# Performance work log

Hardware: AMD Instinct MI355X
Metric: run time of the kernel (lower is better)

## Reference

```python
import jax, jax.numpy as jnp
import numpy as np
from jax import lax

K = 5          # dynamic kernel size
GROUPS = 8     # inter_channels // group_channels = 128 // 16
R = 2          # pixel shuffle upscale factor
SLOPE = 0.01   # LeakyReLU default negative_slope
EPS = 1e-5     # BatchNorm eps


def conv2d(x, w, b, pad=0):
    # x: [B,C,H,W], w: [O,I,kh,kw]
    y = lax.conv_general_dilated(x, w, (1, 1), [(pad, pad), (pad, pad)],
                                 dimension_numbers=('NCHW', 'OIHW', 'NCHW'))
    return y + b[None, :, None, None]


def pixel_shuffle(x, r):
    B, C, H, W = x.shape
    x = x.reshape(B, C // (r * r), r, r, H, W)
    x = x.transpose(0, 1, 4, 2, 5, 3)  # B, C', H, r, W, r
    return x.reshape(B, C // (r * r), H * r, W * r)


def involution(x, weight, k, groups, pad):
    # x: [B,C,H,W]; weight: [B,groups,k,k,H,W]
    # out[b, g*gc+c, h, w] = sum_ij weight[b,g,i,j,h,w] * x_pad[b, g*gc+c, h+i, w+j]
    B, C, H, W = x.shape
    gc = C // groups
    xp = jnp.pad(x, ((0, 0), (0, 0), (pad, pad), (pad, pad)))
    xg = xp.reshape(B, groups, gc, H + 2 * pad, W + 2 * pad)
    out = jnp.zeros((B, groups, gc, H, W), x.dtype)
    for i in range(k):
        for j in range(k):
            out = out + weight[:, :, None, i, j] * xg[:, :, :, i:i + H, j:j + W]
    return out.reshape(B, C, H, W)


def setup_inputs() -> dict:
    key = jax.random.key(0)
    ks = jax.random.split(key, 16)
    s = 0.05
    return {
        'high_level': jax.random.normal(ks[0], (8, 128, 64, 64), jnp.float32),
        'low_level': jax.random.normal(ks[1], (8, 224, 128, 128), jnp.float32),
        'emb': jax.random.normal(ks[2], (8, 256, 128, 128), jnp.float32),
        'reduce_w': jax.random.normal(ks[3], (128, 256, 1, 1), jnp.float32) * s,
        'reduce_b': jax.random.normal(ks[4], (128,), jnp.float32) * s,
        'conv1_w': jax.random.normal(ks[5], (32, 128, 1, 1), jnp.float32) * s,
        'conv1_b': jax.random.normal(ks[6], (32,), jnp.float32) * s,
        'conv2_w': jax.random.normal(ks[7], (200, 32, 3, 3), jnp.float32) * s,
        'conv2_b': jax.random.normal(ks[8], (200,), jnp.float32) * s,
        'embconv_w': jax.random.normal(ks[9], (32, 256, 1, 1), jnp.float32) * s,
        'embconv_b': jax.random.normal(ks[10], (32,), jnp.float32) * s,
        'out_w': jax.random.normal(ks[11], (64, 128, 1, 1), jnp.float32) * s,
        'out_b': jax.random.normal(ks[12], (64,), jnp.float32) * s,
        'bn_gamma': jnp.ones((64,), jnp.float32),
        'bn_beta': jnp.zeros((64,), jnp.float32),
        'bn_mean': jnp.zeros((64,), jnp.float32),
        'bn_var': jax.random.uniform(ks[13], (64,), jnp.float32, 0.5, 1.5),
    }


def reference(high_level, low_level, emb,
              reduce_w, reduce_b, conv1_w, conv1_b, conv2_w, conv2_b,
              embconv_w, embconv_b, out_w, out_b,
              bn_gamma, bn_beta, bn_mean, bn_var):
    cat = jnp.concatenate([pixel_shuffle(high_level, R), low_level], axis=1)
    cat = conv2d(cat, reduce_w, reduce_b)
    mix = jax.nn.leaky_relu(conv2d(cat, conv1_w, conv1_b)
                            + conv2d(emb, embconv_w, embconv_b), SLOPE)
    w = conv2d(mix, conv2_w, conv2_b, pad=1)  # [B, K*K*GROUPS, H, W]
    B, _, H, W = w.shape
    w = w.reshape(B, GROUPS, K, K, H, W)
    o = involution(cat, w, K, GROUPS, (K - 1) // 2)
    o = conv2d(o, out_w, out_b)
    o = (o - bn_mean[None, :, None, None]) * (bn_gamma[None, :, None, None]
        / jnp.sqrt(bn_var[None, :, None, None] + EPS)) + bn_beta[None, :, None, None]
    return jax.nn.leaky_relu(o, SLOPE)
```

## Files before the change

kernel.cpp:

```cpp
#include <hip/hip_runtime.h>

typedef unsigned short u16; typedef unsigned int u32; typedef unsigned long long u64;
typedef __attribute__((ext_vector_type(8))) short short8;
typedef __attribute__((ext_vector_type(16))) float f32x16;

#define HW 16384

#define RED_B  0
#define C1E_B  128
#define C2_B   160
#define OUT_B  416
#define BN_SC  480
#define BN_SH  544
#define FLAG_OFF   4096
#define RWB_OFF    8192
#define C1B_OFF    73728
#define EMBB_OFF   81920
#define OUTB_OFF   98304
#define C2PB_OFF   114688
#define WEFF_OFF   262144
#define CAT2_OFF   524288
#define MIX_OFF    34078720

__device__ __forceinline__ float bf2f(u16 x){ u32 u=((u32)x)<<16; float f; __builtin_memcpy(&f,&u,4); return f; }
__device__ __forceinline__ u16 f2bf(float f){ u32 u; __builtin_memcpy(&u,&f,4); return (u16)((u + 0x7fffu + ((u>>16)&1u))>>16); }
__device__ __forceinline__ u32 pk2(float a, float b){ return (u32)f2bf(a) | ((u32)f2bf(b)<<16); }
__device__ __forceinline__ float lrelu(float x){ return x>0.f ? x : 0.01f*x; }

template<int M> __device__ __forceinline__ u16 ldb(const void* p, size_t i){
    if (M==1) return ((const u16*)p)[i];
    return f2bf(((const float*)p)[i]);
}
template<int M> __device__ __forceinline__ float ldf(const void* p, size_t i){
    if (M==1) return bf2f(((const u16*)p)[i]);
    return ((const float*)p)[i];
}
__device__ __forceinline__ int swz(int p){ return ((p>>1) ^ (p>>3)) & 7; }

__device__ __forceinline__ void gl16(const void* g, void* l){
    __builtin_amdgcn_global_load_lds(
        (const __attribute__((address_space(1))) u32*)g,
        (__attribute__((address_space(3))) u32*)l, 16, 0, 0);
}

__global__ void detect_kernel(const void* __restrict__ emb, u32* __restrict__ flag){
    int tid = threadIdx.x;
    const u16* p = (const u16*)emb;
    int e = (p[tid*2] >> 7) & 0xFF;
    u64 m = __ballot(e >= 100 && e <= 140);
    if (tid == 0) *flag = (__popcll(m) >= 32) ? 1u : 0u;
}

template<int M>
__device__ __forceinline__ void prep_body(
    const void* rw, const void* rb, const void* c1w, const void* c1b,
    const void* c2w, const void* c2b, const void* ew, const void* eb,
    const void* ow, const void* ob, const void* gam, const void* bet,
    const void* mn, const void* vr, char* ws)
{
    float* wf = (float*)ws;
    int i = blockIdx.x*256 + threadIdx.x;
    if (i < 32768) {
        int o = i>>8, ic = i&255;
        int s = ic>>4, qq = (ic>>3)&1, e = ic&7;
        int dst = (((o>>5)*16 + s)*64 + qq*32 + (o&31))*8 + e;
        ((u16*)(ws+RWB_OFF))[dst] = ldb<M>(rw, i);
    }
    else if (i < 36864)  ((u16*)(ws+C1B_OFF))[i-32768] = ldb<M>(c1w, i-32768);
    else if (i < 45056)  ((u16*)(ws+EMBB_OFF))[i-36864] = ldb<M>(ew, i-36864);
    else if (i < 53248)  ((u16*)(ws+OUTB_OFF))[i-45056] = ldb<M>(ow, i-45056);
    else if (i < 126976) {
        int j = i-53248; int o = j/288, k = j - o*288;
        int tap = k>>5, ic = k&31;
        u16 v = 0;
        if (o < 200) v = ldb<M>(c2w, (size_t)o*288 + ic*9 + tap);
        ((u16*)(ws+C2PB_OFF))[j] = v;
    }
    else if (i < 127584) {
        int j = i-126976;
        if (j < 128) wf[RED_B+j] = ldf<M>(rb, j);
        else if (j < 160) {
            int o = j-128;
            float s = ldf<M>(c1b,o) + ldf<M>(eb,o);
#pragma unroll 8
            for (int ic=0; ic<128; ic++)
                s += ldf<M>(c1w, (size_t)o*128+ic) * ldf<M>(rb, ic);
            wf[C1E_B+o] = s;
        }
        else if (j < 416) { int o = j-160; wf[C2_B+o] = (o<200) ? ldf<M>(c2b,o) : 0.f; }
        else if (j < 480) wf[OUT_B+j-416] = ldf<M>(ob, j-416);
        else if (j < 544) { int c=j-480; wf[BN_SC+c] = ldf<M>(gam,c) * rsqrtf(ldf<M>(vr,c)+1e-5f); }
        else { int c=j-544; wf[BN_SH+c] = ldf<M>(bet,c) - ldf<M>(mn,c)*ldf<M>(gam,c)*rsqrtf(ldf<M>(vr,c)+1e-5f); }
    }
    else if (i < 135776) {
        int j = i - 127584; int oc = j>>8, k2 = j&255;
        float s = 0.f;
#pragma unroll 8
        for (int ic=0; ic<128; ic++)
            s += ldf<M>(c1w, (size_t)oc*128+ic) * ldf<M>(rw, (size_t)ic*256+k2);
        ((u16*)(ws+WEFF_OFF))[oc*256+k2] = f2bf(s);
    }
}

__global__ __launch_bounds__(256) void k_prep(
    const void* rw, const void* rb, const void* c1w, const void* c1b,
    const void* c2w, const void* c2b, const void* ew, const void* eb,
    const void* ow, const void* ob, const void* gam, const void* bet,
    const void* mn, const void* vr, char* ws, const u32* __restrict__ flag)
{
    if (*flag) prep_body<1>(rw,rb,c1w,c1b,c2w,c2b,ew,eb,ow,ob,gam,bet,mn,vr,ws);
    else       prep_body<0>(rw,rb,c1w,c1b,c2w,c2b,ew,eb,ow,ob,gam,bet,mn,vr,ws);
}

__global__ __launch_bounds__(512) void k_rm(
    const void* __restrict__ hi, const void* __restrict__ lo, const void* __restrict__ emb,
    const u16* __restrict__ rwB, const u16* __restrict__ weffB, const u16* __restrict__ embB,
    const float* __restrict__ wf, u16* __restrict__ cat2, u16* __restrict__ mixt,
    const u32* __restrict__ flag)
{
    if (*flag != 1u) return;
    __shared__ u16 At1[64*264];
    __shared__ u16 At2[64*264];
    __shared__ u16 raw[34816];

    const int tid = threadIdx.x, wvi = tid>>6, lane = tid&63;
    const int col = lane&31, q = lane>>5;
    const int gpx = blockIdx.x*64;
    const int b = gpx>>14, p0 = gpx&16383;
    const int h = p0>>7, w0 = p0&127;

    {
        for (int i=wvi; i<28; i+=8){
            int chunk = i*64 + lane;
            int ch = chunk>>3, p8 = chunk&7;
            gl16((const u16*)lo + ((size_t)(b*224+ch))*HW + p0 + p8*8,
                 (char*)raw + i*1024);
        }
        {
            int i = wvi;
            int chunk = i*64 + lane;
            int hc = chunk>>2, c4 = chunk&3;
            gl16((const u16*)hi + ((size_t)(b*128+hc))*4096 + (size_t)(h>>1)*64 + (w0>>1) + c4*8,
                 (char*)raw + 28672 + i*1024);
        }
        for (int i=wvi; i<32; i+=8){
            int chunk = i*64 + lane;
            int ch = chunk>>3, p8 = chunk&7;
            gl16((const u16*)emb + ((size_t)(b*256+ch))*HW + p0 + p8*8,
                 (char*)raw + 36864 + i*1024);
        }
    }
    __syncthreads();

    {
        const int sthr = tid & 255;
        const int co = sthr>>3, po = sthr&7;
        u32 W[8][4];
        if (tid >= 256) {
            u32 R[8][4];
#pragma unroll
            for (int j=0;j<8;j++)
                __builtin_memcpy(&R[j][0], raw + 18432 + (8*co+j)*64 + po*8, 16);
#pragma unroll
            for (int p=0;p<8;p++){
                const int u = p>>1, hf = p&1;
#pragma unroll
                for (int m=0;m<4;m++){
                    u32 A0 = R[2*m][u], A1 = R[2*m+1][u];
                    W[p][m] = hf ? ((A0>>16) | (A1 & 0xffff0000u))
                                 : ((A0 & 0xffffu) | (A1<<16));
                }
            }
#pragma unroll
            for (int p=0;p<8;p++){
                int pg = 8*po + p;
                __builtin_memcpy(At2 + pg*264 + ((co ^ swz(pg))<<3), &W[p][0], 16);
            }
        } else if (co >= 4) {
            u32 R[8][4];
#pragma unroll
            for (int j=0;j<8;j++)
                __builtin_memcpy(&R[j][0], raw + (8*(co-4)+j)*64 + po*8, 16);
#pragma unroll
            for (int p=0;p<8;p++){
                const int u = p>>1, hf = p&1;
#pragma unroll
                for (int m=0;m<4;m++){
                    u32 A0 = R[2*m][u], A1 = R[2*m+1][u];
                    W[p][m] = hf ? ((A0>>16) | (A1 & 0xffff0000u))
                                 : ((A0 & 0xffffu) | (A1<<16));
                }
            }
#pragma unroll
            for (int p=0;p<8;p++){
                int pg = 8*po + p;
                __builtin_memcpy(At1 + pg*264 + ((co ^ swz(pg))<<3), &W[p][0], 16);
            }
        } else {
            const int h2 = (h&1)*2;
            u32 E[8][2], O[8][2];
#pragma unroll
            for (int j=0;j<8;j++){
                int hc = (8*co+j)*4 + h2;
                __builtin_memcpy(&E[j][0], raw + 14336 + hc*32 + po*4, 8);
                __builtin_memcpy(&O[j][0], raw + 14336 + (hc+1)*32 + po*4, 8);
            }
#pragma unroll
            for (int p=0;p<8;p++){
                const int k = p>>1, u = k>>1, hf = k&1;
#pragma unroll
                for (int m=0;m<4;m++){
                    u32 A0, A1;
                    if (p&1){ A0 = O[2*m][u]; A1 = O[2*m+1][u]; }
                    else    { A0 = E[2*m][u]; A1 = E[2*m+1][u]; }
                    W[p][m] = hf ? ((A0>>16) | (A1 & 0xffff0000u))
                                 : ((A0 & 0xffffu) | (A1<<16));
                }
            }
#pragma unroll
            for (int p=0;p<8;p++){
                int pg = 8*po + p;
                __builtin_memcpy(At1 + pg*264 + ((co ^ swz(pg))<<3), &W[p][0], 16);
            }
        }
    }
    __syncthreads();

    const int pt = wvi>>2, ks = wvi&3;
    const int pp = pt*32 + col, sw = swz(pp);
    const u16* arow1 = At1 + pp*264;
    const u16* arow2 = At2 + pp*264;

    f32x16 racc, macc;
#pragma unroll
    for (int r=0;r<16;r++){ racc[r]=0.f; macc[r]=0.f; }

    short8 Wf[4], Be2[4];
#pragma unroll
    for (int t4=0;t4<4;t4++)
        __builtin_memcpy(&Wf[t4], weffB + (size_t)col*256 + (4*ks+t4)*16 + q*8, 16);
#pragma unroll
    for (int t4=0;t4<4;t4++)
        __builtin_memcpy(&Be2[t4], embB + (size_t)col*256 + (4*ks+t4)*16 + q*8, 16);

#pragma unroll
    for (int bt=0; bt<4; bt++){
        short8 Bb[4];
#pragma unroll
        for (int si=0;si<4;si++)
            __builtin_memcpy(&Bb[si], rwB + (((size_t)(ks*16 + bt*4 + si))*64 + lane)*8, 16);
#pragma unroll
        for (int si=0;si<4;si++){
            int s = bt*4 + si;
            short8 a; __builtin_memcpy(&a, arow1 + (((2*s+q)^sw)<<3), 16);
            racc = __builtin_amdgcn_mfma_f32_32x32x16_bf16(a, Bb[si], racc, 0,0,0);
            int d = s - 4*ks;
            if (d>=0 && d<4)
                macc = __builtin_amdgcn_mfma_f32_32x32x16_bf16(a, Wf[d], macc, 0,0,0);
        }
    }
#pragma unroll
    for (int t4=0;t4<4;t4++){
        int t = 4*ks + t4;
        short8 a; __builtin_memcpy(&a, arow2 + (((2*t+q)^sw)<<3), 16);
        macc = __builtin_amdgcn_mfma_f32_32x32x16_bf16(a, Be2[t4], macc, 0,0,0);
    }
    {
        int oc = ks*32 + col;
        float bias = wf[RED_B + oc];
#pragma unroll
        for (int r=0;r<16;r++){
            int row = (r&3) + 8*(r>>2) + 4*q;
            cat2[((size_t)(gpx + pt*32 + row))*128 + oc] = f2bf(racc[r] + bias);
        }
    }

    float* exch = (float*)raw;
    if (ks != 0){
#pragma unroll
        for (int r=0;r<16;r++){
            int row = (r&3) + 8*(r>>2) + 4*q;
            exch[pt*3072 + (ks-1)*1024 + row*32 + col] = macc[r];
        }
    }
    __syncthreads();
    if (ks == 0){
        float bias = wf[C1E_B + col];
#pragma unroll
        for (int r=0;r<16;r++){
            int row = (r&3) + 8*(r>>2) + 4*q;
            int base = pt*3072 + row*32 + col;
            float v = macc[r] + exch[base] + exch[base+1024] + exch[base+2048] + bias;
            mixt[((size_t)(gpx + pt*32 + row))*32 + col] = f2bf(lrelu(v));
        }
    }
}

template<int M>
__device__ __forceinline__ void rm_body_reg(
    const void* __restrict__ hi, const void* __restrict__ lo, const void* __restrict__ emb,
    const u16* __restrict__ rwB, const u16* __restrict__ weffB, const u16* __restrict__ embB,
    const float* __restrict__ wf, u16* __restrict__ cat2, u16* __restrict__ mixt,
    u16* At)
{
    const int tid = threadIdx.x, wvi = tid>>6, lane = tid&63;
    const int col = lane&31, q = lane>>5;
    const int gpx = blockIdx.x*64;
    const int b = gpx>>14, p0 = gpx&16383;
    const int h = p0>>7, w0 = p0&127;

    const int sthr = tid & 255;
    const int co = sthr>>3, po = sthr&7;
    const bool is_emb = tid >= 256;

    u32 Wreg[8][4];

    if (is_emb) {
        u32 R[8][4];
        size_t base = ((size_t)(b*256 + 8*co))*HW + p0 + 8*po;
        float raw[8][8];
#pragma unroll
        for (int j=0;j<8;j++)
            __builtin_memcpy(&raw[j][0], (const float*)emb + base + (size_t)j*HW, 32);
#pragma unroll
        for (int j=0;j<8;j++)
#pragma unroll
        for (int m=0;m<4;m++) R[j][m] = pk2(raw[j][2*m], raw[j][2*m+1]);
#pragma unroll
        for (int p=0;p<8;p++){
            const int u = p>>1, hf = p&1;
#pragma unroll
            for (int m=0;m<4;m++){
                u32 A0 = R[2*m][u], A1 = R[2*m+1][u];
                Wreg[p][m] = hf ? ((A0>>16) | (A1 & 0xffff0000u))
                                : ((A0 & 0xffffu) | (A1<<16));
            }
        }
    } else {
        u32 W[8][4];
        if (co < 28) {
            u32 R[8][4];
            size_t base = ((size_t)(b*224 + 8*co))*HW + p0 + 8*po;
            float raw[8][8];
#pragma unroll
            for (int j=0;j<8;j++)
                __builtin_memcpy(&raw[j][0], (const float*)lo + base + (size_t)j*HW, 32);
#pragma unroll
            for (int j=0;j<8;j++)
#pragma unroll
            for (int m=0;m<4;m++) R[j][m] = pk2(raw[j][2*m], raw[j][2*m+1]);
#pragma unroll
            for (int p=0;p<8;p++){
                const int u = p>>1, hf = p&1;
#pragma unroll
                for (int m=0;m<4;m++){
                    u32 A0 = R[2*m][u], A1 = R[2*m+1][u];
                    W[p][m] = hf ? ((A0>>16) | (A1 & 0xffff0000u))
                                 : ((A0 & 0xffffu) | (A1<<16));
                }
            }
            const int ch = co + 4;
#pragma unroll
            for (int p=0;p<8;p++){
                int pg = 8*po + p;
                __builtin_memcpy(At + pg*264 + ((ch ^ swz(pg))<<3), &W[p][0], 16);
            }
        } else {
            const int cc0 = (co-28)*8, h2 = (h&1)*2;
            u32 E[8][2], O[8][2];
            float rE[8][4], rO[8][4];
#pragma unroll
            for (int j=0;j<8;j++){
                int hc = (cc0+j)*4 + h2;
                size_t src = ((size_t)(b*128 + hc))*4096 + (size_t)(h>>1)*64 + (w0>>1) + 4*po;
                __builtin_memcpy(&rE[j][0], (const float*)hi + src, 16);
                __builtin_memcpy(&rO[j][0], (const float*)hi + src + 4096, 16);
            }
#pragma unroll
            for (int j=0;j<8;j++){
                E[j][0] = pk2(rE[j][0], rE[j][1]); E[j][1] = pk2(rE[j][2], rE[j][3]);
                O[j][0] = pk2(rO[j][0], rO[j][1]); O[j][1] = pk2(rO[j][2], rO[j][3]);
            }
#pragma unroll
            for (int p=0;p<8;p++){
                const int k = p>>1, u = k>>1, hf = k&1;
#pragma unroll
                for (int m=0;m<4;m++){
                    u32 A0, A1;
                    if (p&1){ A0 = O[2*m][u]; A1 = O[2*m+1][u]; }
                    else    { A0 = E[2*m][u]; A1 = E[2*m+1][u]; }
                    W[p][m] = hf ? ((A0>>16) | (A1 & 0xffff0000u))
                                 : ((A0 & 0xffffu) | (A1<<16));
                }
            }
            const int ch = co - 28;
#pragma unroll
            for (int p=0;p<8;p++){
                int pg = 8*po + p;
                __builtin_memcpy(At + pg*264 + ((ch ^ swz(pg))<<3), &W[p][0], 16);
            }
        }
    }
    __syncthreads();

    const int pt = wvi>>2, ks = wvi&3;
    const int pp = pt*32 + col, sw = swz(pp);
    const u16* arow = At + pp*264;

    f32x16 racc, macc;
#pragma unroll
    for (int r=0;r<16;r++){ racc[r]=0.f; macc[r]=0.f; }

    short8 Wf[4];
#pragma unroll
    for (int t4=0;t4<4;t4++)
        __builtin_memcpy(&Wf[t4], weffB + (size_t)col*256 + (4*ks+t4)*16 + q*8, 16);

#pragma unroll
    for (int bt=0; bt<4; bt++){
        short8 Bb[4];
#pragma unroll
        for (int si=0;si<4;si++)
            __builtin_memcpy(&Bb[si], rwB + (((size_t)(ks*16 + bt*4 + si))*64 + lane)*8, 16);
#pragma unroll
        for (int si=0;si<4;si++){
            int s = bt*4 + si;
            short8 a; __builtin_memcpy(&a, arow + (((2*s+q)^sw)<<3), 16);
            racc = __builtin_amdgcn_mfma_f32_32x32x16_bf16(a, Bb[si], racc, 0,0,0);
            int d = s - 4*ks;
            if (d>=0 && d<4)
                macc = __builtin_amdgcn_mfma_f32_32x32x16_bf16(a, Wf[d], macc, 0,0,0);
        }
    }
    {
        int oc = ks*32 + col;
        float bias = wf[RED_B + oc];
#pragma unroll
        for (int r=0;r<16;r++){
            int row = (r&3) + 8*(r>>2) + 4*q;
            cat2[((size_t)(gpx + pt*32 + row))*128 + oc] = f2bf(racc[r] + bias);
        }
    }
    __syncthreads();

    if (is_emb){
#pragma unroll
        for (int p=0;p<8;p++){
            int pg = 8*po + p;
            __builtin_memcpy(At + pg*264 + ((co ^ swz(pg))<<3), &Wreg[p][0], 16);
        }
    }
    __syncthreads();

    {
        short8 Be[4];
#pragma unroll
        for (int t4=0;t4<4;t4++)
            __builtin_memcpy(&Be[t4], embB + (size_t)col*256 + (4*ks+t4)*16 + q*8, 16);
#pragma unroll
        for (int t4=0;t4<4;t4++){
            int t = 4*ks + t4;
            short8 a; __builtin_memcpy(&a, arow + (((2*t+q)^sw)<<3), 16);
            macc = __builtin_amdgcn_mfma_f32_32x32x16_bf16(a, Be[t4], macc, 0,0,0);
        }
    }
    __syncthreads();

    float* exch = (float*)At;
    if (ks != 0){
#pragma unroll
        for (int r=0;r<16;r++){
            int row = (r&3) + 8*(r>>2) + 4*q;
            exch[pt*3072 + (ks-1)*1024 + row*32 + col] = macc[r];
        }
    }
    __syncthreads();
    if (ks == 0){
        float bias = wf[C1E_B + col];
#pragma unroll
        for (int r=0;r<16;r++){
            int row = (r&3) + 8*(r>>2) + 4*q;
            int base = pt*3072 + row*32 + col;
            float v = macc[r] + exch[base] + exch[base+1024] + exch[base+2048] + bias;
            mixt[((size_t)(gpx + pt*32 + row))*32 + col] = f2bf(lrelu(v));
        }
    }
}

__global__ __launch_bounds__(512,4) void k_rmf(
    const void* __restrict__ hi, const void* __restrict__ lo, const void* __restrict__ emb,
    const u16* __restrict__ rwB, const u16* __restrict__ weffB, const u16* __restrict__ embB,
    const float* __restrict__ wf, u16* __restrict__ cat2, u16* __restrict__ mixt,
    const u32* __restrict__ flag)
{
    if (*flag != 0u) return;
    __shared__ u16 At[64*264];
    rm_body_reg<0>(hi, lo, emb, rwB, weffB, embB, wf, cat2, mixt, At);
}

template<int M>
__device__ __forceinline__ void inv_body(
    const u16* __restrict__ cat2, const u16* __restrict__ mixt,
    const u16* __restrict__ c2B, const u16* __restrict__ outB,
    const float* __restrict__ wf, void* __restrict__ out,
    u16* halo_m, u16* wgt_l, u16* halo_c, u16* og)
{
    const int tid = threadIdx.x, wvi = tid>>6, lane = tid&63;
    const int col = lane&31, q = lane>>5;
    const int b = blockIdx.y, ty = blockIdx.x>>3, tx = blockIdx.x&7;
    const int py = tid>>4, px = tid&15;

    f32x16 acc[2][2];
#pragma unroll
    for (int i=0;i<2;i++)
#pragma unroll
    for (int j=0;j<2;j++)
#pragma unroll
    for (int r=0;r<16;r++) acc[i][j][r] = 0.f;

#pragma unroll
    for (int i=0;i<6;i++){
        int idx = tid + i*256;
        if (idx < 1296){
            int point = idx>>2, cq = idx&3;
            int y = ty*16 + point/18 - 1, x = tx*16 + point%18 - 1;
            short8 v;
            if (y>=0 && y<128 && x>=0 && x<128)
                __builtin_memcpy(&v, mixt + ((size_t)(b*HW + y*128 + x))*32 + cq*8, 16);
            else { short z=0; v = (short8){z,z,z,z,z,z,z,z}; }
            *(short8*)(halo_m + point*40 + cq*8) = v;
        }
    }
    __syncthreads();

#pragma unroll 1
    for (int g=0; g<8; g++){
        __syncthreads();

        const int o = g*25 + col;
        short8 Bf[18];
#pragma unroll
        for (int s=0;s<18;s++)
            __builtin_memcpy(&Bf[s], c2B + (size_t)o*288 + s*16 + q*8, 16);

#pragma unroll
        for (int i=0;i<4;i++){
            int idx = tid + i*256;
            if (idx < 800){
                int point = idx>>1, cq = idx&1;
                int y = ty*16 + point/20 - 2, x = tx*16 + point%20 - 2;
                short8 v;
                if (y>=0 && y<128 && x>=0 && x<128)
                    __builtin_memcpy(&v, cat2 + ((size_t)(b*HW + y*128 + x))*128 + g*16 + cq*8, 16);
                else { short z=0; v = (short8){z,z,z,z,z,z,z,z}; }
                *(short8*)(halo_c + point*16 + cq*8) = v;
            }
        }

        f32x16 c0, c1;
#pragma unroll
        for (int r=0;r<16;r++){ c0[r]=0.f; c1[r]=0.f; }
        const int p0 = wvi*64 + col, p1 = p0 + 32;
        const int pya = p0>>4, pxa = p0&15, pyb = p1>>4, pxb = p1&15;
#pragma unroll
        for (int s=0;s<18;s++){
            int tap = s>>1, ih = s&1;
            int dy = tap/3, dx = tap%3;
            short8 a0, a1;
            __builtin_memcpy(&a0, halo_m + ((pya+dy)*18 + pxa+dx)*40 + ih*16 + q*8, 16);
            __builtin_memcpy(&a1, halo_m + ((pyb+dy)*18 + pxb+dx)*40 + ih*16 + q*8, 16);
            c0 = __builtin_amdgcn_mfma_f32_32x32x16_bf16(a0, Bf[s], c0, 0,0,0);
            c1 = __builtin_amdgcn_mfma_f32_32x32x16_bf16(a1, Bf[s], c1, 0,0,0);
        }
        {
            float bias = wf[C2_B + o];
#pragma unroll
            for (int rt2=0; rt2<2; rt2++){
                int mb = wvi*64 + rt2*32;
#pragma unroll
                for (int r=0;r<16;r+=2){
                    int row0 = (r&3) + 8*(r>>2) + 4*q;
                    float v0 = (rt2 ? c1[r]   : c0[r])   + bias;
                    float v1 = (rt2 ? c1[r+1] : c0[r+1]) + bias;
                    u32 pkv = (u32)f2bf(v0) | ((u32)f2bf(v1)<<16);
                    *(u32*)(wgt_l + (size_t)col*264 + mb + row0) = pkv;
                }
            }
        }
        __syncthreads();

        float wvv[25];
#pragma unroll
        for (int t=0;t<25;t++) wvv[t] = bf2f(wgt_l[t*264 + tid]);

        float a16[16];
#pragma unroll
        for (int cc=0;cc<16;cc++) a16[cc]=0.f;
#pragma unroll
        for (int t=0;t<25;t++){
            int dy = t/5, dx = t%5;
            u32 vv[8];
            __builtin_memcpy(vv, halo_c + ((py+dy)*20 + px+dx)*16, 32);
            float wt = wvv[t];
#pragma unroll
            for (int r=0;r<8;r++){
                u32 u = vv[r];
                u32 ulo = u<<16, uhi = u & 0xffff0000u;
                float x0, x1;
                __builtin_memcpy(&x0,&ulo,4); __builtin_memcpy(&x1,&uhi,4);
                a16[2*r]   += wt*x0;
                a16[2*r+1] += wt*x1;
            }
        }
        u32 pk[8];
#pragma unroll
        for (int r=0;r<8;r++) pk[r] = (u32)f2bf(a16[2*r]) | ((u32)f2bf(a16[2*r+1])<<16);
        __builtin_memcpy(og + tid*16, pk, 32);
        __syncthreads();

        short8 bo0, bo1;
        __builtin_memcpy(&bo0, outB + (size_t)(col)*128      + g*16 + q*8, 16);
        __builtin_memcpy(&bo1, outB + (size_t)(32+col)*128   + g*16 + q*8, 16);
#pragma unroll
        for (int rt2=0; rt2<2; rt2++){
            int prow = (wvi*2 + rt2)*32 + col;
            short8 a; __builtin_memcpy(&a, og + prow*16 + q*8, 16);
            acc[rt2][0] = __builtin_amdgcn_mfma_f32_32x32x16_bf16(a, bo0, acc[rt2][0], 0,0,0);
            acc[rt2][1] = __builtin_amdgcn_mfma_f32_32x32x16_bf16(a, bo1, acc[rt2][1], 0,0,0);
        }
    }
#pragma unroll
    for (int rt2=0; rt2<2; rt2++)
#pragma unroll
    for (int nt=0; nt<2; nt++){
        int oc = nt*32 + col;
        float bias = wf[OUT_B+oc], sc = wf[BN_SC+oc], sh = wf[BN_SH+oc];
#pragma unroll
        for (int r=0;r<16;r++){
            int row = (r&3) + 8*(r>>2) + 4*q;
            int p = (wvi*2 + rt2)*32 + row;
            int yy = ty*16 + (p>>4), xx = tx*16 + (p&15);
            float v = lrelu((acc[rt2][nt][r] + bias)*sc + sh);
            size_t oidx = ((size_t)(b*64 + oc))*HW + yy*128 + xx;
            if (M==1) ((u16*)out)[oidx] = f2bf(v);
            else ((float*)out)[oidx] = v;
        }
    }
}

__global__ __launch_bounds__(256,2) void k_inv(
    const u16* __restrict__ cat2, const u16* __restrict__ mixt,
    const u16* __restrict__ c2B, const u16* __restrict__ outB,
    const float* __restrict__ wf, void* __restrict__ out, const u32* __restrict__ flag)
{
    __shared__ u16 halo_m[324*40];
    __shared__ u16 wgt_l[32*264];
    __shared__ u16 halo_c[400*16];
    __shared__ u16 og[256*16];
    if (*flag) inv_body<1>(cat2, mixt, c2B, outB, wf, out, halo_m, wgt_l, halo_c, og);
    else       inv_body<0>(cat2, mixt, c2B, outB, wf, out, halo_m, wgt_l, halo_c, og);
}

extern "C" void kernel_launch(void* const* d_in, const int* in_sizes, int n_in,
                              void* d_out, int out_size, void* d_ws, size_t ws_size,
                              hipStream_t stream) {
    const void* hi  = d_in[0];
    const void* lo  = d_in[1];
    const void* emb = d_in[2];
    char* ws = (char*)d_ws;
    float* wf = (float*)ws;
    u32* flag = (u32*)(ws + FLAG_OFF);
    u16* cat2 = (u16*)(ws + CAT2_OFF);
    u16* mixt = (u16*)(ws + MIX_OFF);

    detect_kernel<<<1, 64, 0, stream>>>(emb, flag);

    k_prep<<<531,256,0,stream>>>(d_in[3],d_in[4],d_in[5],d_in[6],d_in[7],d_in[8],
        d_in[9],d_in[10],d_in[11],d_in[12],d_in[13],d_in[14],d_in[15],d_in[16], ws, flag);

    k_rm<<<2048,512,0,stream>>>(hi, lo, emb, (const u16*)(ws+RWB_OFF),
                                (const u16*)(ws+WEFF_OFF), (const u16*)(ws+EMBB_OFF),
                                wf, cat2, mixt, flag);
    k_rmf<<<2048,512,0,stream>>>(hi, lo, emb, (const u16*)(ws+RWB_OFF),
                                 (const u16*)(ws+WEFF_OFF), (const u16*)(ws+EMBB_OFF),
                                 wf, cat2, mixt, flag);

    k_inv<<<dim3(64,8),256,0,stream>>>(cat2, mixt, (const u16*)(ws+C2PB_OFF),
                                       (const u16*)(ws+OUTB_OFF), wf, d_out, flag);
}
```

Baseline: 431.1 us.

## Stage k_rmf input loads through LDS with async global-to-shared copies

Result: no change. 428.8 us (-0.5%).

```diff
diff --git a/kernel.cpp b/kernel.cpp
--- a/kernel.cpp
+++ b/kernel.cpp
@@ -112,6 +112,185 @@
     else       prep_body<0>(rw,rb,c1w,c1b,c2w,c2b,ew,eb,ow,ob,gam,bet,mn,vr,ws);
 }
 
+__device__ __forceinline__ void trans_half_f32(
+    const float* rowbase, int rstart, int po, int jh, u16* At, int chunkIdx)
+{
+    u32 R2[4][4];
+#pragma unroll
+    for (int jp=0;jp<4;jp++){
+        int r = rstart + 4*jh + jp;
+        int v = (r>>2)&15;
+        float fa[4], fb[4];
+        __builtin_memcpy(fa, rowbase + r*64 + ((2*po)^v)*4, 16);
+        __builtin_memcpy(fb, rowbase + r*64 + ((2*po+1)^v)*4, 16);
+        R2[jp][0]=pk2(fa[0],fa[1]); R2[jp][1]=pk2(fa[2],fa[3]);
+        R2[jp][2]=pk2(fb[0],fb[1]); R2[jp][3]=pk2(fb[2],fb[3]);
+    }
+#pragma unroll
+    for (int p=0;p<8;p++){
+        const int u=p>>1, hf=p&1;
+        u32 Wh[2];
+#pragma unroll
+        for (int mp=0;mp<2;mp++){
+            u32 A0=R2[2*mp][u], A1=R2[2*mp+1][u];
+            Wh[mp] = hf ? ((A0>>16)|(A1&0xffff0000u)) : ((A0&0xffffu)|(A1<<16));
+        }
+        int pg = 8*po+p;
+        __builtin_memcpy(At + pg*264 + ((chunkIdx ^ swz(pg))<<3) + jh*4, Wh, 8);
+    }
+}
+
+__global__ __launch_bounds__(512) void k_rmf(
+    const void* __restrict__ hi, const void* __restrict__ lo, const void* __restrict__ emb,
+    const u16* __restrict__ rwB, const u16* __restrict__ weffB, const u16* __restrict__ embB,
+    const float* __restrict__ wf, u16* __restrict__ cat2, u16* __restrict__ mixt,
+    const u32* __restrict__ flag)
+{
+    if (*flag != 0u) return;
+    __shared__ float rawf[18432];
+    __shared__ u16 At[64*264];
+
+    const int tid = threadIdx.x, wvi = tid>>6, lane = tid&63;
+    const int col = lane&31, q = lane>>5;
+    const int gpx = blockIdx.x*64;
+    const int b = gpx>>14, p0 = gpx&16383;
+    const int h = p0>>7, w0 = p0&127;
+
+    for (int i=wvi; i<56; i+=8){
+        int r = 4*i + (lane>>4);
+        int qd = (lane&15) ^ (i&15);
+        gl16((const float*)lo + ((size_t)(b*224 + r))*HW + p0 + qd*4,
+             (char*)rawf + i*1024);
+    }
+    for (int i=wvi; i<16; i+=8){
+        int hc = 8*i + (lane>>3);
+        int qd = (lane&7) ^ (i&7);
+        gl16((const float*)hi + ((size_t)(b*128 + hc))*4096 + (size_t)(h>>1)*64 + (w0>>1) + qd*4,
+             (char*)rawf + 57344 + i*1024);
+    }
+    __syncthreads();
+
+    {
+        const int co = tid>>4, po = (tid>>1)&7, jh = tid&1;
+        if (co >= 4) {
+            trans_half_f32(rawf, 8*(co-4), po, jh, At, co);
+        } else {
+            const int h2 = (h&1)*2;
+            u32 E2[4][2], O2[4][2];
+#pragma unroll
+            for (int jp=0;jp<4;jp++){
+                int hc = (8*co + 4*jh + jp)*4 + h2;
+                int slot = po ^ ((hc>>3)&7);
+                float fe[4], fo[4];
+                __builtin_memcpy(fe, rawf + 14336 + hc*32 + slot*4, 16);
+                __builtin_memcpy(fo, rawf + 14336 + (hc+1)*32 + slot*4, 16);
+                E2[jp][0]=pk2(fe[0],fe[1]); E2[jp][1]=pk2(fe[2],fe[3]);
+                O2[jp][0]=pk2(fo[0],fo[1]); O2[jp][1]=pk2(fo[2],fo[3]);
+            }
+#pragma unroll
+            for (int p=0;p<8;p++){
+                const int k=p>>1, u=k>>1, hf=k&1;
+                u32 Wh[2];
+#pragma unroll
+                for (int mp=0;mp<2;mp++){
+                    u32 A0 = (p&1) ? O2[2*mp][u] : E2[2*mp][u];
+                    u32 A1 = (p&1) ? O2[2*mp+1][u] : E2[2*mp+1][u];
+                    Wh[mp] = hf ? ((A0>>16)|(A1&0xffff0000u)) : ((A0&0xffffu)|(A1<<16));
+                }
+                int pg = 8*po+p;
+                __builtin_memcpy(At + pg*264 + ((co ^ swz(pg))<<3) + jh*4, Wh, 8);
+            }
+        }
+    }
+    __syncthreads();
+
+    for (int i=wvi; i<64; i+=8){
+        int r = 4*i + (lane>>4);
+        int qd = (lane&15) ^ (i&15);
+        gl16((const float*)emb + ((size_t)(b*256 + r))*HW + p0 + qd*4,
+             (char*)rawf + i*1024);
+    }
+
+    const int pt = wvi>>2, ks = wvi&3;
+    const int pp = pt*32 + col, sw = swz(pp);
+    const u16* arow = At + pp*264;
+
+    f32x16 racc, macc;
+#pragma unroll
+    for (int r=0;r<16;r++){ racc[r]=0.f; macc[r]=0.f; }
+
+    short8 Wf[4];
+#pragma unroll
+    for (int t4=0;t4<4;t4++)
+        __builtin_memcpy(&Wf[t4], weffB + (size_t)col*256 + (4*ks+t4)*16 + q*8, 16);
+
+#pragma unroll
+    for (int bt=0; bt<4; bt++){
+        short8 Bb[4];
+#pragma unroll
+        for (int si=0;si<4;si++)
+            __builtin_memcpy(&Bb[si], rwB + (((size_t)(ks*16 + bt*4 + si))*64 + lane)*8, 16);
+#pragma unroll
+        for (int si=0;si<4;si++){
+            int s = bt*4 + si;
+            short8 a; __builtin_memcpy(&a, arow + (((2*s+q)^sw)<<3), 16);
+            racc = __builtin_amdgcn_mfma_f32_32x32x16_bf16(a, Bb[si], racc, 0,0,0);
+            int d = s - 4*ks;
+            if (d>=0 && d<4)
+                macc = __builtin_amdgcn_mfma_f32_32x32x16_bf16(a, Wf[d], macc, 0,0,0);
+        }
+    }
+    {
+        int oc = ks*32 + col;
+        float bias = wf[RED_B + oc];
+#pragma unroll
+        for (int r=0;r<16;r++){
+            int row = (r&3) + 8*(r>>2) + 4*q;
+            cat2[((size_t)(gpx + pt*32 + row))*128 + oc] = f2bf(racc[r] + bias);
+        }
+    }
+    __syncthreads();
+
+    {
+        const int co = tid>>4, po = (tid>>1)&7, jh = tid&1;
+        trans_half_f32(rawf, 8*co, po, jh, At, co);
+    }
+    __syncthreads();
+
+    {
+        short8 Be[4];
+#pragma unroll
+        for (int t4=0;t4<4;t4++)
+            __builtin_memcpy(&Be[t4], embB + (size_t)col*256 + (4*ks+t4)*16 + q*8, 16);
+#pragma unroll
+        for (int t4=0;t4<4;t4++){
+            int t = 4*ks + t4;
+            short8 a; __builtin_memcpy(&a, arow + (((2*t+q)^sw)<<3), 16);
+            macc = __builtin_amdgcn_mfma_f32_32x32x16_bf16(a, Be[t4], macc, 0,0,0);
+        }
+    }
+
+    float* exch = rawf;
+    if (ks != 0){
+#pragma unroll
+        for (int r=0;r<16;r++){
+            int row = (r&3) + 8*(r>>2) + 4*q;
+            exch[pt*3072 + (ks-1)*1024 + row*32 + col] = macc[r];
+        }
+    }
+    __syncthreads();
+    if (ks == 0){
+        float bias = wf[C1E_B + col];
+#pragma unroll
+        for (int r=0;r<16;r++){
+            int row = (r&3) + 8*(r>>2) + 4*q;
+            int base = pt*3072 + row*32 + col;
+            float v = macc[r] + exch[base] + exch[base+1024] + exch[base+2048] + bias;
+            mixt[((size_t)(gpx + pt*32 + row))*32 + col] = f2bf(lrelu(v));
+        }
+    }
+}
+
 __global__ __launch_bounds__(512) void k_rm(
     const void* __restrict__ hi, const void* __restrict__ lo, const void* __restrict__ emb,
     const u16* __restrict__ rwB, const u16* __restrict__ weffB, const u16* __restrict__ embB,
@@ -294,208 +473,6 @@
             mixt[((size_t)(gpx + pt*32 + row))*32 + col] = f2bf(lrelu(v));
         }
     }
-}
-
-template<int M>
-__device__ __forceinline__ void rm_body_reg(
-    const void* __restrict__ hi, const void* __restrict__ lo, const void* __restrict__ emb,
-    const u16* __restrict__ rwB, const u16* __restrict__ weffB, const u16* __restrict__ embB,
-    const float* __restrict__ wf, u16* __restrict__ cat2, u16* __restrict__ mixt,
-    u16* At)
-{
-    const int tid = threadIdx.x, wvi = tid>>6, lane = tid&63;
-    const int col = lane&31, q = lane>>5;
-    const int gpx = blockIdx.x*64;
-    const int b = gpx>>14, p0 = gpx&16383;
-    const int h = p0>>7, w0 = p0&127;
-
-    const int sthr = tid & 255;
-    const int co = sthr>>3, po = sthr&7;
-    const bool is_emb = tid >= 256;
-
-    u32 Wreg[8][4];
-
-    if (is_emb) {
-        u32 R[8][4];
-        size_t base = ((size_t)(b*256 + 8*co))*HW + p0 + 8*po;
-        float raw[8][8];
-#pragma unroll
-        for (int j=0;j<8;j++)
-            __builtin_memcpy(&raw[j][0], (const float*)emb + base + (size_t)j*HW, 32);
-#pragma unroll
-        for (int j=0;j<8;j++)
-#pragma unroll
-        for (int m=0;m<4;m++) R[j][m] = pk2(raw[j][2*m], raw[j][2*m+1]);
-#pragma unroll
-        for (int p=0;p<8;p++){
-            const int u = p>>1, hf = p&1;
-#pragma unroll
-            for (int m=0;m<4;m++){
-                u32 A0 = R[2*m][u], A1 = R[2*m+1][u];
-                Wreg[p][m] = hf ? ((A0>>16) | (A1 & 0xffff0000u))
-                                : ((A0 & 0xffffu) | (A1<<16));
-            }
-        }
-    } else {
-        u32 W[8][4];
-        if (co < 28) {
-            u32 R[8][4];
-            size_t base = ((size_t)(b*224 + 8*co))*HW + p0 + 8*po;
-            float raw[8][8];
-#pragma unroll
-            for (int j=0;j<8;j++)
-                __builtin_memcpy(&raw[j][0], (const float*)lo + base + (size_t)j*HW, 32);
-#pragma unroll
-            for (int j=0;j<8;j++)
-#pragma unroll
-            for (int m=0;m<4;m++) R[j][m] = pk2(raw[j][2*m], raw[j][2*m+1]);
-#pragma unroll
-            for (int p=0;p<8;p++){
-                const int u = p>>1, hf = p&1;
-#pragma unroll
-                for (int m=0;m<4;m++){
-                    u32 A0 = R[2*m][u], A1 = R[2*m+1][u];
-                    W[p][m] = hf ? ((A0>>16) | (A1 & 0xffff0000u))
-                                 : ((A0 & 0xffffu) | (A1<<16));
-                }
-            }
-            const int ch = co + 4;
-#pragma unroll
-            for (int p=0;p<8;p++){
-                int pg = 8*po + p;
-                __builtin_memcpy(At + pg*264 + ((ch ^ swz(pg))<<3), &W[p][0], 16);
-            }
-        } else {
-            const int cc0 = (co-28)*8, h2 = (h&1)*2;
-            u32 E[8][2], O[8][2];
-            float rE[8][4], rO[8][4];
-#pragma unroll
-            for (int j=0;j<8;j++){
-                int hc = (cc0+j)*4 + h2;
-                size_t src = ((size_t)(b*128 + hc))*4096 + (size_t)(h>>1)*64 + (w0>>1) + 4*po;
-                __builtin_memcpy(&rE[j][0], (const float*)hi + src, 16);
-                __builtin_memcpy(&rO[j][0], (const float*)hi + src + 4096, 16);
-            }
-#pragma unroll
-            for (int j=0;j<8;j++){
-                E[j][0] = pk2(rE[j][0], rE[j][1]); E[j][1] = pk2(rE[j][2], rE[j][3]);
-                O[j][0] = pk2(rO[j][0], rO[j][1]); O[j][1] = pk2(rO[j][2], rO[j][3]);
-            }
-#pragma unroll
-            for (int p=0;p<8;p++){
-                const int k = p>>1, u = k>>1, hf = k&1;
-#pragma unroll
-                for (int m=0;m<4;m++){
-                    u32 A0, A1;
-                    if (p&1){ A0 = O[2*m][u]; A1 = O[2*m+1][u]; }
-                    else    { A0 = E[2*m][u]; A1 = E[2*m+1][u]; }
-                    W[p][m] = hf ? ((A0>>16) | (A1 & 0xffff0000u))
-                                 : ((A0 & 0xffffu) | (A1<<16));
-                }
-            }
-            const int ch = co - 28;
-#pragma unroll
-            for (int p=0;p<8;p++){
-                int pg = 8*po + p;
-                __builtin_memcpy(At + pg*264 + ((ch ^ swz(pg))<<3), &W[p][0], 16);
-            }
-        }
-    }
-    __syncthreads();
-
-    const int pt = wvi>>2, ks = wvi&3;
-    const int pp = pt*32 + col, sw = swz(pp);
-    const u16* arow = At + pp*264;
-
-    f32x16 racc, macc;
-#pragma unroll
-    for (int r=0;r<16;r++){ racc[r]=0.f; macc[r]=0.f; }
-
-    short8 Wf[4];
-#pragma unroll
-    for (int t4=0;t4<4;t4++)
-        __builtin_memcpy(&Wf[t4], weffB + (size_t)col*256 + (4*ks+t4)*16 + q*8, 16);
-
-#pragma unroll
-    for (int bt=0; bt<4; bt++){
-        short8 Bb[4];
-#pragma unroll
-        for (int si=0;si<4;si++)
-            __builtin_memcpy(&Bb[si], rwB + (((size_t)(ks*16 + bt*4 + si))*64 + lane)*8, 16);
-#pragma unroll
-        for (int si=0;si<4;si++){
-            int s = bt*4 + si;
-            short8 a; __builtin_memcpy(&a, arow + (((2*s+q)^sw)<<3), 16);
-            racc = __builtin_amdgcn_mfma_f32_32x32x16_bf16(a, Bb[si], racc, 0,0,0);
-            int d = s - 4*ks;
-            if (d>=0 && d<4)
-                macc = __builtin_amdgcn_mfma_f32_32x32x16_bf16(a, Wf[d], macc, 0,0,0);
-        }
-    }
-    {
-        int oc = ks*32 + col;
-        float bias = wf[RED_B + oc];
-#pragma unroll
-        for (int r=0;r<16;r++){
-            int row = (r&3) + 8*(r>>2) + 4*q;
-            cat2[((size_t)(gpx + pt*32 + row))*128 + oc] = f2bf(racc[r] + bias);
-        }
-    }
-    __syncthreads();
-
-    if (is_emb){
-#pragma unroll
-        for (int p=0;p<8;p++){
-            int pg = 8*po + p;
-            __builtin_memcpy(At + pg*264 + ((co ^ swz(pg))<<3), &Wreg[p][0], 16);
-        }
-    }
-    __syncthreads();
-
-    {
-        short8 Be[4];
-#pragma unroll
-        for (int t4=0;t4<4;t4++)
-            __builtin_memcpy(&Be[t4], embB + (size_t)col*256 + (4*ks+t4)*16 + q*8, 16);
-#pragma unroll
-        for (int t4=0;t4<4;t4++){
-            int t = 4*ks + t4;
-            short8 a; __builtin_memcpy(&a, arow + (((2*t+q)^sw)<<3), 16);
-            macc = __builtin_amdgcn_mfma_f32_32x32x16_bf16(a, Be[t4], macc, 0,0,0);
-        }
-    }
-    __syncthreads();
-
-    float* exch = (float*)At;
-    if (ks != 0){
-#pragma unroll
-        for (int r=0;r<16;r++){
-            int row = (r&3) + 8*(r>>2) + 4*q;
-            exch[pt*3072 + (ks-1)*1024 + row*32 + col] = macc[r];
-        }
-    }
-    __syncthreads();
-    if (ks == 0){
-        float bias = wf[C1E_B + col];
-#pragma unroll
-        for (int r=0;r<16;r++){
-            int row = (r&3) + 8*(r>>2) + 4*q;
-            int base = pt*3072 + row*32 + col;
-            float v = macc[r] + exch[base] + exch[base+1024] + exch[base+2048] + bias;
-            mixt[((size_t)(gpx + pt*32 + row))*32 + col] = f2bf(lrelu(v));
-        }
-    }
-}
-
-__global__ __launch_bounds__(512,4) void k_rmf(
-    const void* __restrict__ hi, const void* __restrict__ lo, const void* __restrict__ emb,
-    const u16* __restrict__ rwB, const u16* __restrict__ weffB, const u16* __restrict__ embB,
-    const float* __restrict__ wf, u16* __restrict__ cat2, u16* __restrict__ mixt,
-    const u32* __restrict__ flag)
-{
-    if (*flag != 0u) return;
-    __shared__ u16 At[64*264];
-    rm_body_reg<0>(hi, lo, emb, rwB, weffB, embB, wf, cat2, mixt, At);
 }
 
 template<int M>
@@ -678,12 +655,12 @@
     k_prep<<<531,256,0,stream>>>(d_in[3],d_in[4],d_in[5],d_in[6],d_in[7],d_in[8],
         d_in[9],d_in[10],d_in[11],d_in[12],d_in[13],d_in[14],d_in[15],d_in[16], ws, flag);
 
+    k_rmf<<<2048,512,0,stream>>>(hi, lo, emb, (const u16*)(ws+RWB_OFF),
+                                 (const u16*)(ws+WEFF_OFF), (const u16*)(ws+EMBB_OFF),
+                                 wf, cat2, mixt, flag);
     k_rm<<<2048,512,0,stream>>>(hi, lo, emb, (const u16*)(ws+RWB_OFF),
                                 (const u16*)(ws+WEFF_OFF), (const u16*)(ws+EMBB_OFF),
                                 wf, cat2, mixt, flag);
-    k_rmf<<<2048,512,0,stream>>>(hi, lo, emb, (const u16*)(ws+RWB_OFF),
-                                 (const u16*)(ws+WEFF_OFF), (const u16*)(ws+EMBB_OFF),
-                                 wf, cat2, mixt, flag);
 
     k_inv<<<dim3(64,8),256,0,stream>>>(cat2, mixt, (const u16*)(ws+C2PB_OFF),
                                        (const u16*)(ws+OUTB_OFF), wf, d_out, flag);
```
